# Kernel tuning notes

Measured on AMD Instinct MI355X. Metric: run time of the kernel, lower is better.

Reference implementation:

```python
import jax, jax.numpy as jnp
import numpy as np

NUM_CLASSES = 80
STRIDES = (8, 16, 32)


def _decode(p, stride):
    # p: [B, 5+C, H, W] raw head -> [B, HW, 5+C] decoded (xy in px, wh=exp*stride)
    B, C, H, W = p.shape
    ys, xs = jnp.meshgrid(jnp.arange(H), jnp.arange(W), indexing='ij')
    grid = jnp.stack([xs, ys], -1).reshape(H * W, 2).astype(p.dtype)
    out = p.reshape(B, C, H * W).transpose(0, 2, 1)
    xy = (out[..., :2] + grid) * stride
    wh = jnp.exp(out[..., 2:4]) * stride
    out = jnp.concatenate([xy, wh, out[..., 4:]], -1)
    es = jnp.full((H * W,), float(stride), p.dtype)
    return out, grid[:, 0], grid[:, 1], es


def _pairwise_iou(gt, pr):
    # gt [G,4] cxcywh, pr [A,4] -> [G,A]
    gt_tl = gt[:, None, :2] - gt[:, None, 2:] * 0.5
    gt_br = gt[:, None, :2] + gt[:, None, 2:] * 0.5
    pr_tl = pr[None, :, :2] - pr[None, :, 2:] * 0.5
    pr_br = pr[None, :, :2] + pr[None, :, 2:] * 0.5
    tl = jnp.maximum(gt_tl, pr_tl)
    br = jnp.minimum(gt_br, pr_br)
    en = jnp.all(tl < br, -1).astype(gt.dtype)
    inter = jnp.prod(br - tl, -1) * en
    a_gt = jnp.prod(gt[:, 2:], -1)[:, None]
    a_pr = jnp.prod(pr[:, 2:], -1)[None, :]
    return inter / (a_gt + a_pr - inter + 1e-16)


def _assign(gt_boxes, gt_cls, bbox, clsp, objp, xg, yg, es):
    # SimOTA assignment for one image (all fixed-shape; non-candidate anchors
    # are masked out via huge cost instead of boolean gather).
    G = gt_boxes.shape[0]
    xc = (xg + 0.5) * es  # [A] anchor centers
    yc = (yg + 0.5) * es
    gl = gt_boxes[:, 0:1] - 0.5 * gt_boxes[:, 2:3]
    gr = gt_boxes[:, 0:1] + 0.5 * gt_boxes[:, 2:3]
    gt_ = gt_boxes[:, 1:2] - 0.5 * gt_boxes[:, 3:4]
    gb = gt_boxes[:, 1:2] + 0.5 * gt_boxes[:, 3:4]
    in_box = (xc[None] > gl) & (xc[None] < gr) & (yc[None] > gt_) & (yc[None] < gb)  # [G,A]
    r = 2.5 * es[None]
    in_ctr = ((xc[None] > gt_boxes[:, 0:1] - r) & (xc[None] < gt_boxes[:, 0:1] + r)
              & (yc[None] > gt_boxes[:, 1:2] - r) & (yc[None] < gt_boxes[:, 1:2] + r))
    fg_cand = jnp.any(in_box, 0) | jnp.any(in_ctr, 0)  # [A]
    in_both = in_box & in_ctr  # [G,A]

    ious = _pairwise_iou(gt_boxes, bbox)  # [G,A]
    ious_m = jnp.where(fg_cand[None, :], ious, 0.0)
    iou_cost = -jnp.log(ious_m + 1e-8)

    # pairwise cls BCE cost: bce(sqrt(sigmoid(cls)*sigmoid(obj)), onehot(gt)).sum(-1)
    p = jnp.sqrt(jax.nn.sigmoid(clsp) * jax.nn.sigmoid(objp[:, None]))  # [A,C]
    lp = jnp.maximum(jnp.log(p), -100.0)
    l1p = jnp.maximum(jnp.log1p(-p), -100.0)
    t = jax.nn.one_hot(gt_cls, NUM_CLASSES, dtype=p.dtype)  # [G,C]
    cls_cost = -(jnp.einsum('ac,gc->ga', lp - l1p, t) + jnp.sum(l1p, -1)[None, :])

    cost = (cls_cost + 3.0 * iou_cost
            + 1e5 * (~in_both).astype(p.dtype)
            + 1e9 * (~fg_cand)[None, :].astype(p.dtype))

    # dynamic-k: k_g = clamp(sum(top10 ious), min=1)
    topk_ious, _ = jax.lax.top_k(ious_m, 10)
    dyn_k = jnp.clip(topk_ious.sum(-1).astype(jnp.int32), 1, None)  # [G]
    rank = jnp.argsort(jnp.argsort(cost, axis=1), axis=1)  # rank of each anchor per gt
    matching = (rank < dyn_k[:, None]) & fg_cand[None, :]  # [G,A]
    # resolve anchors matched to multiple gts: keep min-cost gt
    multi = matching.sum(0) > 1
    best = jnp.argmin(cost, 0)
    matching = jnp.where(multi[None, :], jnp.arange(G)[:, None] == best[None, :], matching)

    fg = jnp.any(matching, 0)  # [A]
    matched_gt = jnp.argmax(matching, 0)  # [A]
    pred_iou = jnp.sum(matching * ious, 0)  # [A]
    matched_cls = gt_cls[matched_gt]
    return fg, matched_gt, pred_iou, matched_cls


def _giou_loss(b, g):
    tl = jnp.maximum(b[..., :2] - b[..., 2:] * 0.5, g[..., :2] - g[..., 2:] * 0.5)
    br = jnp.minimum(b[..., :2] + b[..., 2:] * 0.5, g[..., :2] + g[..., 2:] * 0.5)
    area_b = jnp.prod(b[..., 2:], -1)
    area_g = jnp.prod(g[..., 2:], -1)
    en = jnp.all(tl < br, -1).astype(b.dtype)
    inter = jnp.prod(br - tl, -1) * en
    union = area_b + area_g - inter
    iou = inter / (union + 1e-16)
    ctl = jnp.minimum(b[..., :2] - b[..., 2:] * 0.5, g[..., :2] - g[..., 2:] * 0.5)
    cbr = jnp.maximum(b[..., :2] + b[..., 2:] * 0.5, g[..., :2] + g[..., 2:] * 0.5)
    area_c = jnp.maximum(jnp.prod(cbr - ctl, -1), 1e-16)
    giou = iou - (area_c - union) / area_c
    return 1.0 - jnp.clip(giou, -1.0, 1.0)


def _bce_logits(x, t):
    return jnp.maximum(x, 0.0) - x * t + jnp.log1p(jnp.exp(-jnp.abs(x)))


def _forward(p8, p16, p32, labels):
    outs, xo, yo, eo = [], [], [], []
    for p, s in zip((p8, p16, p32), STRIDES):
        o, x, y, e = _decode(p, s)
        outs.append(o); xo.append(x); yo.append(y); eo.append(e)
    outputs = jnp.concatenate(outs, 1)  # [B, A, 5+C]
    xg = jnp.concatenate(xo); yg = jnp.concatenate(yo); es = jnp.concatenate(eo)

    bbox = outputs[..., :4]
    obj = outputs[..., 4]
    cls = outputs[..., 5:]
    gt_boxes = labels[..., :4]
    gt_cls = labels[..., 4].astype(jnp.int32)

    # assignment runs under no_grad in torch
    det = jax.lax.stop_gradient(outputs)
    fg, matched_gt, pred_iou, matched_cls = jax.vmap(
        lambda gb, gc, o: _assign(gb, gc, o[..., :4], o[..., 5:], o[..., 4], xg, yg, es)
    )(gt_boxes, gt_cls, det)

    fgf = fg.astype(outputs.dtype)  # [B,A]
    reg_t = jnp.take_along_axis(gt_boxes, matched_gt[..., None], axis=1)  # [B,A,4]
    cls_t = (jax.nn.one_hot(matched_cls, NUM_CLASSES, dtype=outputs.dtype)
             * pred_iou[..., None] * fgf[..., None])

    loss_iou = jnp.sum(_giou_loss(bbox, reg_t) * fgf)
    loss_obj = jnp.sum(_bce_logits(obj, fgf))
    loss_cls = jnp.sum(_bce_logits(cls, cls_t) * fgf[..., None])
    num_fg = jnp.maximum(jnp.sum(fgf), 1.0)
    return (5.0 * loss_iou + loss_obj + loss_cls) / num_fg


def setup_inputs() -> dict:
    key = jax.random.key(0)
    k1, k2, k3, k4, k5, k6 = jax.random.split(key, 6)
    B, NGT = 32, 20
    p8 = jax.random.normal(k1, (B, 5 + NUM_CLASSES, 80, 80), dtype=jnp.float32)
    p16 = jax.random.normal(k2, (B, 5 + NUM_CLASSES, 40, 40), dtype=jnp.float32)
    p32 = jax.random.normal(k3, (B, 5 + NUM_CLASSES, 20, 20), dtype=jnp.float32)
    cxy = jax.random.uniform(k4, (B, NGT, 2), dtype=jnp.float32, minval=32.0, maxval=608.0)
    wh = jax.random.uniform(k5, (B, NGT, 2), dtype=jnp.float32, minval=16.0, maxval=128.0)
    cls = jax.random.randint(k6, (B, NGT, 1), 0, NUM_CLASSES).astype(jnp.float32)
    labels = jnp.concatenate([cxy, wh, cls], -1)
    return {"p8": p8, "p16": p16, "p32": p32, "labels": labels}


def reference(p8, p16, p32, labels):
    return _forward(p8, p16, p32, labels)
```

## Files before the change

kernel.cpp:

```cpp
#include <hip/hip_runtime.h>
#include <cstdint>
#include <cstddef>

#define NA 8400
#define NAP 8448
#define NB 32
#define NG 20
#define NCL 80
#define NBLK 33
#define KC_BLKS 12

__device__ __forceinline__ float frcp(float x) { return __builtin_amdgcn_rcpf(x); }
__device__ __forceinline__ float bce0(float x) {
  return fmaxf(x, 0.0f) + __logf(1.0f + __expf(-fabsf(x)));
}

__device__ __forceinline__ void anchor_info(int a, const float* p8, const float* p16,
                                            const float* p32, int b, const float*& base,
                                            int& hw, int& HW, int& xg, int& yg, float& fs) {
  if (a < 6400)      { hw = a;        HW = 6400; xg = hw % 80; yg = hw / 80; fs = 8.f;
                       base = p8  + (size_t)b * 85 * 6400; }
  else if (a < 8000) { hw = a - 6400; HW = 1600; xg = hw % 40; yg = hw / 40; fs = 16.f;
                       base = p16 + (size_t)b * 85 * 1600; }
  else               { hw = a - 8000; HW = 400;  xg = hw % 20; yg = hw / 20; fs = 32.f;
                       base = p32 + (size_t)b * 85 * 400; }
}

__device__ __forceinline__ float iou_raw(float gx, float gy, float gw, float gh, float4 p) {
  float gtlx = gx - gw * 0.5f, gtly = gy - gh * 0.5f;
  float gbrx = gx + gw * 0.5f, gbry = gy + gh * 0.5f;
  float ptlx = p.x - p.z * 0.5f, ptly = p.y - p.w * 0.5f;
  float pbrx = p.x + p.z * 0.5f, pbry = p.y + p.w * 0.5f;
  float tlx = fmaxf(gtlx, ptlx), tly = fmaxf(gtly, ptly);
  float brx = fminf(gbrx, pbrx), bry = fminf(gbry, pbry);
  float inter = ((tlx < brx) && (tly < bry)) ? (brx - tlx) * (bry - tly) : 0.0f;
  float ag = gw * gh, ap = p.z * p.w;
  return inter * frcp(ag + ap - inter + 1e-16f);
}

__device__ __forceinline__ float giou_loss(float4 bb, float gx, float gy, float gw, float gh) {
  float btlx = bb.x - bb.z * 0.5f, btly = bb.y - bb.w * 0.5f;
  float bbrx = bb.x + bb.z * 0.5f, bbry = bb.y + bb.w * 0.5f;
  float gtlx = gx - gw * 0.5f, gtly = gy - gh * 0.5f;
  float gbrx = gx + gw * 0.5f, gbry = gy + gh * 0.5f;
  float tlx = fmaxf(btlx, gtlx), tly = fmaxf(btly, gtly);
  float brx = fminf(bbrx, gbrx), bry = fminf(bbry, gbry);
  float area_b = bb.z * bb.w, area_g = gw * gh;
  float inter = ((tlx < brx) && (tly < bry)) ? (brx - tlx) * (bry - tly) : 0.0f;
  float uni = area_b + area_g - inter;
  float iou = inter / (uni + 1e-16f);
  float ctlx = fminf(btlx, gtlx), ctly = fminf(btly, gtly);
  float cbrx = fmaxf(bbrx, gbrx), cbry = fmaxf(bbry, gbry);
  float area_c = fmaxf((cbrx - ctlx) * (cbry - ctly), 1e-16f);
  float giou = iou - (area_c - uni) / area_c;
  giou = fminf(fmaxf(giou, -1.0f), 1.0f);
  return 1.0f - giou;
}

__device__ __forceinline__ void block_argmin(float& v, int& i, volatile float* s_v,
                                             volatile int* s_i, int tid) {
#pragma unroll
  for (int off = 32; off; off >>= 1) {
    float ov = __shfl_down(v, off, 64);
    int   oi = __shfl_down(i, off, 64);
    if (ov < v || (ov == v && oi < i)) { v = ov; i = oi; }
  }
  if ((tid & 63) == 0) { s_v[tid >> 6] = v; s_i[tid >> 6] = i; }
  __syncthreads();
  v = s_v[0]; i = s_i[0];
#pragma unroll
  for (int w = 1; w < 4; ++w) {
    float ov = s_v[w]; int oi = s_i[w];
    if (ov < v || (ov == v && oi < i)) { v = ov; i = oi; }
  }
}

__global__ __launch_bounds__(256) void kGXA(const float* __restrict__ p8,
                                            const float* __restrict__ p16,
                                            const float* __restrict__ p32,
                                            const float* __restrict__ labels,
                                            int* __restrict__ n_fg_cnt,
                                            int* __restrict__ fg_list,
                                            float4* __restrict__ bbox_c,
                                            float* __restrict__ sb_c,
                                            float* __restrict__ cost_tbl,
                                            float* __restrict__ iou_tbl,
                                            unsigned int* __restrict__ match_c,
                                            float* __restrict__ blk_obj) {
  __shared__ float s_gt[NG * 4];
  __shared__ int   s_gcls[NG];
  __shared__ int   s_a[256];
  __shared__ unsigned int s_msk[256];
  __shared__ float s_lso[256];
  __shared__ unsigned int s_wcnt[4];
  __shared__ float s_part[4];
  __shared__ unsigned int s_base;
  __shared__ int s_c;
  int blk = blockIdx.x, b = blockIdx.y, tid = threadIdx.x, lane = tid & 63, wid = tid >> 6;

  if (tid < NG) {
    s_gt[tid * 4 + 0] = labels[((size_t)b * NG + tid) * 5 + 0];
    s_gt[tid * 4 + 1] = labels[((size_t)b * NG + tid) * 5 + 1];
    s_gt[tid * 4 + 2] = labels[((size_t)b * NG + tid) * 5 + 2];
    s_gt[tid * 4 + 3] = labels[((size_t)b * NG + tid) * 5 + 3];
    s_gcls[tid] = (int)labels[((size_t)b * NG + tid) * 5 + 4];
  }
  __syncthreads();

  int a = blk * 256 + tid;
  match_c[(size_t)b * NAP + a] = 0u;

  bool fg = false;
  unsigned int msk = 0u;
  float bce_obj = 0.0f, obj = 0.0f;
  if (a < NA) {
    const float* base; int hw, HW, xg, yg; float fs;
    anchor_info(a, p8, p16, p32, b, base, hw, HW, xg, yg, fs);
    obj = base[4 * HW + hw];
    bce_obj = bce0(obj);
    float xc = ((float)xg + 0.5f) * fs;
    float yc = ((float)yg + 0.5f) * fs;
    float r = 2.5f * fs;
#pragma unroll
    for (int g = 0; g < NG; ++g) {
      float gx = s_gt[g * 4 + 0], gy = s_gt[g * 4 + 1];
      float gw = s_gt[g * 4 + 2], gh = s_gt[g * 4 + 3];
      bool inb = (xc > gx - 0.5f * gw) && (xc < gx + 0.5f * gw) &&
                 (yc > gy - 0.5f * gh) && (yc < gy + 0.5f * gh);
      bool inc = (xc > gx - r) && (xc < gx + r) && (yc > gy - r) && (yc < gy + r);
      fg = fg || inb || inc;
      if (inb && inc) msk |= (1u << g);
    }
  }

  unsigned long long bm = __ballot(fg);
#pragma unroll
  for (int off = 32; off; off >>= 1) bce_obj += __shfl_down(bce_obj, off, 64);
  if (lane == 0) { s_wcnt[wid] = (unsigned int)__popcll(bm); s_part[wid] = bce_obj; }
  __syncthreads();
  if (tid == 0) {
    unsigned int cnt = s_wcnt[0] + s_wcnt[1] + s_wcnt[2] + s_wcnt[3];
    s_c = (int)cnt;
    s_base = cnt ? (unsigned int)atomicAdd(&n_fg_cnt[b], (int)cnt) : 0u;
    blk_obj[b * NBLK + blk] = s_part[0] + s_part[1] + s_part[2] + s_part[3];
  }
  if (fg) {
    unsigned int li = 0;
    for (int w = 0; w < wid; ++w) li += s_wcnt[w];
    li += (unsigned int)__popcll(bm & ((1ull << lane) - 1ull));
    s_a[li] = a;
    s_msk[li] = msk;
    float uo = __logf(1.0f + __expf(-fabsf(obj)));
    s_lso[li] = fminf(obj, 0.0f) - uo;
  }
  __syncthreads();

  int c = s_c;
  if (tid >= c) return;
  int ci = (int)s_base + tid;
  size_t bo = (size_t)b * NAP;
  int aa = s_a[tid];
  unsigned int mk = s_msk[tid];
  float lso = s_lso[tid];

  const float* base; int hw, HW, xg, yg; float fs;
  anchor_info(aa, p8, p16, p32, b, base, hw, HW, xg, yg, fs);
  fg_list[bo + ci] = aa;

  float v0 = base[hw];
  float v1 = base[HW + hw];
  float v2 = base[2 * HW + hw];
  float v3 = base[3 * HW + hw];
  float4 pb = make_float4((v0 + (float)xg) * fs, (v1 + (float)yg) * fs,
                          __expf(v2) * fs, __expf(v3) * fs);
  bbox_c[bo + ci] = pb;

  float sl = 0.0f, sb = 0.0f;
  for (int cc = 0; cc < NCL; cc += 8) {
    float xs[8];
#pragma unroll
    for (int j = 0; j < 8; ++j) xs[j] = base[(5 + cc + j) * HW + hw];
#pragma unroll
    for (int j = 0; j < 8; ++j) {
      float x = xs[j];
      float u = __logf(1.0f + __expf(-fabsf(x)));
      sb += fmaxf(x, 0.0f) + u;
      float lsx = fminf(x, 0.0f) - u;
      float lpr = 0.5f * (lsx + lso);
      float p   = __expf(lpr);
      sl += fmaxf(__logf(1.0f - p), -100.0f);
    }
  }
  sb_c[bo + ci] = sb;

  for (int g = 0; g < NG; ++g) {
    int cg = s_gcls[g];
    float x = base[(5 + cg) * HW + hw];
    float u = __logf(1.0f + __expf(-fabsf(x)));
    float lsx = fminf(x, 0.0f) - u;
    float lpr = 0.5f * (lsx + lso);
    float p   = __expf(lpr);
    float l1p = fmaxf(__logf(1.0f - p), -100.0f);
    float wv  = fmaxf(lpr, -100.0f) - l1p;
    float iou = iou_raw(s_gt[g * 4 + 0], s_gt[g * 4 + 1], s_gt[g * 4 + 2], s_gt[g * 4 + 3], pb);
    float cst = -(wv + sl) - 3.0f * __logf(iou + 1e-8f);
    if (!((mk >> g) & 1u)) cst += 100000.0f;
    size_t row = ((size_t)b * NG + g) * NAP + ci;
    cost_tbl[row] = cst;
    iou_tbl[row]  = iou;
  }
}

__global__ __launch_bounds__(256) void kB(const float* __restrict__ cost_tbl,
                                          const float* __restrict__ iou_tbl,
                                          const int* __restrict__ n_fg,
                                          unsigned int* __restrict__ match_c) {
  __shared__ float s_cost[NAP];
  __shared__ float s_wt[4 * 10];
  __shared__ float s_v[4];
  __shared__ int   s_i[4];
  __shared__ int   s_k;

  int g = blockIdx.x, b = blockIdx.y, tid = threadIdx.x;
  int lane = tid & 63, wid = tid >> 6;
  int n = n_fg[b];
  size_t bo = (size_t)b * NAP;
  const float* __restrict__ cg = cost_tbl + ((size_t)b * NG + g) * NAP;
  const float* __restrict__ ig = iou_tbl  + ((size_t)b * NG + g) * NAP;

  float t10[10];
#pragma unroll
  for (int j = 0; j < 10; ++j) t10[j] = 0.0f;

  for (int ci = tid; ci < n; ci += 256) {
    float iou = ig[ci];
    float cst = cg[ci];
    if (iou > t10[9]) {
      t10[9] = iou;
#pragma unroll
      for (int q = 9; q > 0; --q) {
        if (t10[q] > t10[q - 1]) { float t = t10[q]; t10[q] = t10[q - 1]; t10[q - 1] = t; }
        else break;
      }
    }
    s_cost[ci] = cst;
  }

  for (int r = 0; r < 10; ++r) {
    float v = t10[0];
    float bv = v;
#pragma unroll
    for (int off = 32; off; off >>= 1) bv = fmaxf(bv, __shfl_down(bv, off, 64));
    bv = __shfl(bv, 0, 64);
    unsigned long long won = __ballot(v == bv);
    if (lane == __ffsll(won) - 1) {
#pragma unroll
      for (int q = 0; q < 9; ++q) t10[q] = t10[q + 1];
      t10[9] = -1.0f;
    }
    if (lane == 0) s_wt[wid * 10 + r] = bv;
  }
  __syncthreads();

  if (tid == 0) {
    int p0 = 0, p1 = 0, p2 = 0, p3 = 0;
    float s = 0.0f;
    for (int r = 0; r < 10; ++r) {
      float v0 = (p0 < 10) ? s_wt[p0]      : -2.0f;
      float v1 = (p1 < 10) ? s_wt[10 + p1] : -2.0f;
      float v2 = (p2 < 10) ? s_wt[20 + p2] : -2.0f;
      float v3 = (p3 < 10) ? s_wt[30 + p3] : -2.0f;
      float m = fmaxf(fmaxf(v0, v1), fmaxf(v2, v3));
      s += m;
      if (m == v0) ++p0; else if (m == v1) ++p1; else if (m == v2) ++p2; else ++p3;
    }
    int k = (int)s;
    if (k < 1) k = 1;
    s_k = k;
  }
  __syncthreads();
  int k = s_k;

  for (int it = 0; it < k; ++it) {
    float bv = 3.4e38f; int bi = NAP;
    for (int ci = tid; ci < n; ci += 256) {
      float v = s_cost[ci];
      if (v < bv || (v == bv && ci < bi)) { bv = v; bi = ci; }
    }
    block_argmin(bv, bi, s_v, s_i, tid);
    if (bv >= 1e8f) break;
    if (tid == 0) {
      atomicOr(&match_c[bo + bi], 1u << g);
      s_cost[bi] = 3.4e38f;
    }
    __syncthreads();
  }
}

__global__ __launch_bounds__(256) void kCD(const float* __restrict__ p8,
                                           const float* __restrict__ p16,
                                           const float* __restrict__ p32,
                                           const float* __restrict__ labels,
                                           const float4* __restrict__ bbox_c,
                                           const float* __restrict__ sb_c,
                                           const float* __restrict__ cost_tbl,
                                           const float* __restrict__ iou_tbl,
                                           const int* __restrict__ fg_list,
                                           const int* __restrict__ n_fg,
                                           const unsigned int* __restrict__ match_c,
                                           const float* __restrict__ blk_obj,
                                           float* __restrict__ accum,
                                           int* __restrict__ done_cnt,
                                           float* __restrict__ out) {
  __shared__ float s_gt[NG * 5];
  __shared__ float s_red[16];
  __shared__ int s_last;
  int b = blockIdx.y, tid = threadIdx.x;
  if (tid < NG * 5) s_gt[tid] = labels[(size_t)b * NG * 5 + tid];
  __syncthreads();

  int n = n_fg[b];
  size_t bo = (size_t)b * NAP;
  float li = 0.0f, oe = 0.0f, lc = 0.0f, nf = 0.0f;

  for (int ci = blockIdx.x * 256 + tid; ci < n; ci += KC_BLKS * 256) {
    unsigned int m = match_c[bo + ci];
    if (m == 0u) continue;
    int mg;
    if (m & (m - 1)) {
      float bestc = 3.4e38f; mg = 0;
#pragma unroll 4
      for (int g = 0; g < NG; ++g) {
        float cst = cost_tbl[((size_t)b * NG + g) * NAP + ci];
        if (cst < bestc) { bestc = cst; mg = g; }
      }
    } else {
      mg = __ffs(m) - 1;
    }
    int a = fg_list[bo + ci];
    const float* base; int hw, HW, xg, yg; float fs;
    anchor_info(a, p8, p16, p32, b, base, hw, HW, xg, yg, fs);
    float4 pb = bbox_c[bo + ci];
    float gx = s_gt[mg * 5], gy = s_gt[mg * 5 + 1];
    float gw = s_gt[mg * 5 + 2], gh = s_gt[mg * 5 + 3];
    int cg = (int)s_gt[mg * 5 + 4];
    float piou = iou_tbl[((size_t)b * NG + mg) * NAP + ci];
    li += giou_loss(pb, gx, gy, gw, gh);
    float xcls = base[(5 + cg) * HW + hw];
    lc += sb_c[bo + ci] - xcls * piou;
    oe += base[4 * HW + hw];
    nf += 1.0f;
  }

  float vals[4] = {li, oe, lc, nf};
#pragma unroll
  for (int q = 0; q < 4; ++q) {
#pragma unroll
    for (int off = 32; off; off >>= 1) vals[q] += __shfl_down(vals[q], off, 64);
  }
  if ((tid & 63) == 0) {
    int wid = tid >> 6;
    s_red[wid * 4 + 0] = vals[0];
    s_red[wid * 4 + 1] = vals[1];
    s_red[wid * 4 + 2] = vals[2];
    s_red[wid * 4 + 3] = vals[3];
  }
  __syncthreads();
  if (tid < 4) {
    const int slot[4] = {0, 2, 3, 4};
    float s = s_red[tid] + s_red[4 + tid] + s_red[8 + tid] + s_red[12 + tid];
    atomicAdd(&accum[slot[tid]], s);
  }

  if (tid == 0) {
    __threadfence();
    int old = atomicAdd(done_cnt, 1);
    s_last = (old == KC_BLKS * NB - 1) ? 1 : 0;
  }
  __syncthreads();
  if (s_last) {
    float s = 0.0f;
    for (int i = tid; i < NB * NBLK; i += 256) s += blk_obj[i];
#pragma unroll
    for (int off = 32; off; off >>= 1) s += __shfl_down(s, off, 64);
    if ((tid & 63) == 0) s_red[tid >> 6] = s;
    __syncthreads();
    if (tid == 0) {
      float obj_base = s_red[0] + s_red[1] + s_red[2] + s_red[3];
      float loss_iou = atomicAdd(&accum[0], 0.0f);
      float oex      = atomicAdd(&accum[2], 0.0f);
      float loss_cls = atomicAdd(&accum[3], 0.0f);
      float num_fg   = atomicAdd(&accum[4], 0.0f);
      float loss_obj = obj_base - oex;
      out[0] = (5.0f * loss_iou + loss_obj + loss_cls) / fmaxf(num_fg, 1.0f);
    }
  }
}

extern "C" void kernel_launch(void* const* d_in, const int* in_sizes, int n_in,
                              void* d_out, int out_size, void* d_ws, size_t ws_size,
                              hipStream_t stream) {
  const float* p8     = (const float*)d_in[0];
  const float* p16    = (const float*)d_in[1];
  const float* p32    = (const float*)d_in[2];
  const float* labels = (const float*)d_in[3];
  float* out = (float*)d_out;

  const size_t BAP = (size_t)NB * NAP;
  char* w = (char*)d_ws;
  float4*       bbox_c   = (float4*)w;
  float*        cost_tbl = (float*)(w + BAP * 16);
  float*        iou_tbl  = cost_tbl + (size_t)NB * NG * NAP;
  char*         w2       = (char*)(iou_tbl + (size_t)NB * NG * NAP);
  int*          fg_list  = (int*)(w2);
  unsigned int* match_c  = (unsigned int*)(w2 + BAP * 4);
  float*        sb_c     = (float*)(w2 + BAP * 8);
  char*         w3       = w2 + BAP * 12;
  int*          n_fg     = (int*)w3;
  float*        accum    = (float*)(w3 + 128);
  int*          done_cnt = (int*)(w3 + 160);
  float*        blk_obj  = (float*)(w3 + 256);

  hipMemsetAsync(w3, 0, 256, stream);

  kGXA<<<dim3(NBLK, NB), dim3(256), 0, stream>>>(p8, p16, p32, labels, n_fg, fg_list,
                                                 bbox_c, sb_c, cost_tbl, iou_tbl,
                                                 match_c, blk_obj);
  kB<<<dim3(NG, NB), dim3(256), 0, stream>>>(cost_tbl, iou_tbl, n_fg, match_c);
  kCD<<<dim3(KC_BLKS, NB), dim3(256), 0, stream>>>(p8, p16, p32, labels, bbox_c, sb_c,
                                                   cost_tbl, iou_tbl, fg_list, n_fg,
                                                   match_c, blk_obj, accum, done_cnt, out);
}
```

Baseline: 181.2 us.

## Split fused candidate kernel into compact, class-reduce and per-GT cost kernels

The single candidate-processing kernel is split into three. k1 compacts foreground anchors and stores bbox, log-sigmoid objectness and the in-box mask. k2 spreads the 80-class BCE sums over 8 thread groups per anchor and reduces them through shared memory. k3 computes the cost and IoU tables with one grid slice per ground truth. The aim is to remove load imbalance, since previously only the foreground threads of each block did all the class and GT work serially. The trade-off is two extra launches and extra global round-trips for the intermediate arrays.

```diff
diff --git a/kernel.cpp b/kernel.cpp
--- a/kernel.cpp
+++ b/kernel.cpp
@@ -75,27 +75,21 @@
   }
 }
 
-__global__ __launch_bounds__(256) void kGXA(const float* __restrict__ p8,
-                                            const float* __restrict__ p16,
-                                            const float* __restrict__ p32,
-                                            const float* __restrict__ labels,
-                                            int* __restrict__ n_fg_cnt,
-                                            int* __restrict__ fg_list,
-                                            float4* __restrict__ bbox_c,
-                                            float* __restrict__ sb_c,
-                                            float* __restrict__ cost_tbl,
-                                            float* __restrict__ iou_tbl,
-                                            unsigned int* __restrict__ match_c,
-                                            float* __restrict__ blk_obj) {
+__global__ __launch_bounds__(256) void k1(const float* __restrict__ p8,
+                                          const float* __restrict__ p16,
+                                          const float* __restrict__ p32,
+                                          const float* __restrict__ labels,
+                                          int* __restrict__ n_fg_cnt,
+                                          int* __restrict__ fg_list,
+                                          unsigned int* __restrict__ am_c,
+                                          float4* __restrict__ bbox_c,
+                                          float* __restrict__ lso_c,
+                                          unsigned int* __restrict__ match_c,
+                                          float* __restrict__ blk_obj) {
   __shared__ float s_gt[NG * 4];
-  __shared__ int   s_gcls[NG];
-  __shared__ int   s_a[256];
-  __shared__ unsigned int s_msk[256];
-  __shared__ float s_lso[256];
   __shared__ unsigned int s_wcnt[4];
   __shared__ float s_part[4];
   __shared__ unsigned int s_base;
-  __shared__ int s_c;
   int blk = blockIdx.x, b = blockIdx.y, tid = threadIdx.x, lane = tid & 63, wid = tid >> 6;
 
   if (tid < NG) {
@@ -103,7 +97,6 @@
     s_gt[tid * 4 + 1] = labels[((size_t)b * NG + tid) * 5 + 1];
     s_gt[tid * 4 + 2] = labels[((size_t)b * NG + tid) * 5 + 2];
     s_gt[tid * 4 + 3] = labels[((size_t)b * NG + tid) * 5 + 3];
-    s_gcls[tid] = (int)labels[((size_t)b * NG + tid) * 5 + 4];
   }
   __syncthreads();
 
@@ -113,8 +106,8 @@
   bool fg = false;
   unsigned int msk = 0u;
   float bce_obj = 0.0f, obj = 0.0f;
+  const float* base = nullptr; int hw = 0, HW = 0, xg = 0, yg = 0; float fs = 8.f;
   if (a < NA) {
-    const float* base; int hw, HW, xg, yg; float fs;
     anchor_info(a, p8, p16, p32, b, base, hw, HW, xg, yg, fs);
     obj = base[4 * HW + hw];
     bce_obj = bce0(obj);
@@ -140,74 +133,128 @@
   __syncthreads();
   if (tid == 0) {
     unsigned int cnt = s_wcnt[0] + s_wcnt[1] + s_wcnt[2] + s_wcnt[3];
-    s_c = (int)cnt;
     s_base = cnt ? (unsigned int)atomicAdd(&n_fg_cnt[b], (int)cnt) : 0u;
     blk_obj[b * NBLK + blk] = s_part[0] + s_part[1] + s_part[2] + s_part[3];
   }
-  if (fg) {
-    unsigned int li = 0;
-    for (int w = 0; w < wid; ++w) li += s_wcnt[w];
-    li += (unsigned int)__popcll(bm & ((1ull << lane) - 1ull));
-    s_a[li] = a;
-    s_msk[li] = msk;
-    float uo = __logf(1.0f + __expf(-fabsf(obj)));
-    s_lso[li] = fminf(obj, 0.0f) - uo;
-  }
-  __syncthreads();
-
-  int c = s_c;
-  if (tid >= c) return;
-  int ci = (int)s_base + tid;
+  __syncthreads();
+
+  if (!fg) return;
+  unsigned int pos = s_base;
+  for (int w = 0; w < wid; ++w) pos += s_wcnt[w];
+  pos += (unsigned int)__popcll(bm & ((1ull << lane) - 1ull));
   size_t bo = (size_t)b * NAP;
-  int aa = s_a[tid];
-  unsigned int mk = s_msk[tid];
-  float lso = s_lso[tid];
-
-  const float* base; int hw, HW, xg, yg; float fs;
-  anchor_info(aa, p8, p16, p32, b, base, hw, HW, xg, yg, fs);
-  fg_list[bo + ci] = aa;
+  int ci = (int)pos;
+  fg_list[bo + ci] = a;
+  am_c[bo + ci] = msk;
 
   float v0 = base[hw];
   float v1 = base[HW + hw];
   float v2 = base[2 * HW + hw];
   float v3 = base[3 * HW + hw];
-  float4 pb = make_float4((v0 + (float)xg) * fs, (v1 + (float)yg) * fs,
-                          __expf(v2) * fs, __expf(v3) * fs);
-  bbox_c[bo + ci] = pb;
-
-  float sl = 0.0f, sb = 0.0f;
-  for (int cc = 0; cc < NCL; cc += 8) {
-    float xs[8];
-#pragma unroll
-    for (int j = 0; j < 8; ++j) xs[j] = base[(5 + cc + j) * HW + hw];
-#pragma unroll
-    for (int j = 0; j < 8; ++j) {
-      float x = xs[j];
-      float u = __logf(1.0f + __expf(-fabsf(x)));
-      sb += fmaxf(x, 0.0f) + u;
-      float lsx = fminf(x, 0.0f) - u;
-      float lpr = 0.5f * (lsx + lso);
-      float p   = __expf(lpr);
-      sl += fmaxf(__logf(1.0f - p), -100.0f);
-    }
-  }
-  sb_c[bo + ci] = sb;
-
-  for (int g = 0; g < NG; ++g) {
-    int cg = s_gcls[g];
-    float x = base[(5 + cg) * HW + hw];
+  bbox_c[bo + ci] = make_float4((v0 + (float)xg) * fs, (v1 + (float)yg) * fs,
+                                __expf(v2) * fs, __expf(v3) * fs);
+  float uo = __logf(1.0f + __expf(-fabsf(obj)));
+  lso_c[bo + ci] = fminf(obj, 0.0f) - uo;
+}
+
+__global__ __launch_bounds__(256) void k2(const float* __restrict__ p8,
+                                          const float* __restrict__ p16,
+                                          const float* __restrict__ p32,
+                                          const int* __restrict__ fg_list,
+                                          const int* __restrict__ n_fg,
+                                          const float* __restrict__ lso_c,
+                                          float* __restrict__ sl_c,
+                                          float* __restrict__ sb_c) {
+  __shared__ float s_sl[8][33];
+  __shared__ float s_sb[8][33];
+  int b = blockIdx.y, tid = threadIdx.x;
+  int part = tid >> 5, cl = tid & 31;
+  int n = n_fg[b];
+  size_t bo = (size_t)b * NAP;
+
+  for (int base_ci = blockIdx.x * 32; base_ci < n; base_ci += gridDim.x * 32) {
+    int ci = base_ci + cl;
+    bool act = ci < n;
+    float sl = 0.0f, sb = 0.0f;
+    if (act) {
+      int a = fg_list[bo + ci];
+      float lso = lso_c[bo + ci];
+      const float* base; int hw, HW, xg, yg; float fs;
+      anchor_info(a, p8, p16, p32, b, base, hw, HW, xg, yg, fs);
+      const float* cb = base + (size_t)(5 + part * 10) * HW + hw;
+      float xs[10];
+#pragma unroll
+      for (int j = 0; j < 5; ++j) xs[j] = cb[j * HW];
+#pragma unroll
+      for (int j = 5; j < 10; ++j) xs[j] = cb[j * HW];
+#pragma unroll
+      for (int j = 0; j < 10; ++j) {
+        float x = xs[j];
+        float u = __logf(1.0f + __expf(-fabsf(x)));
+        sb += fmaxf(x, 0.0f) + u;
+        float lsx = fminf(x, 0.0f) - u;
+        float lpr = 0.5f * (lsx + lso);
+        float p   = __expf(lpr);
+        sl += fmaxf(__logf(1.0f - p), -100.0f);
+      }
+    }
+    s_sl[part][cl] = sl;
+    s_sb[part][cl] = sb;
+    __syncthreads();
+    if (tid < 32 && base_ci + tid < n) {
+      float tsl = 0.0f, tsb = 0.0f;
+#pragma unroll
+      for (int q = 0; q < 8; ++q) { tsl += s_sl[q][tid]; tsb += s_sb[q][tid]; }
+      sl_c[bo + base_ci + tid] = tsl;
+      sb_c[bo + base_ci + tid] = tsb;
+    }
+    __syncthreads();
+  }
+}
+
+__global__ __launch_bounds__(256) void k3(const float* __restrict__ p8,
+                                          const float* __restrict__ p16,
+                                          const float* __restrict__ p32,
+                                          const float* __restrict__ labels,
+                                          const int* __restrict__ fg_list,
+                                          const int* __restrict__ n_fg,
+                                          const float* __restrict__ lso_c,
+                                          const float* __restrict__ sl_c,
+                                          const float4* __restrict__ bbox_c,
+                                          const unsigned int* __restrict__ am_c,
+                                          float* __restrict__ cost_tbl,
+                                          float* __restrict__ iou_tbl) {
+  int g = blockIdx.y, b = blockIdx.z, tid = threadIdx.x;
+  int n = n_fg[b];
+  size_t bo = (size_t)b * NAP;
+  float gx = labels[((size_t)b * NG + g) * 5 + 0];
+  float gy = labels[((size_t)b * NG + g) * 5 + 1];
+  float gw = labels[((size_t)b * NG + g) * 5 + 2];
+  float gh = labels[((size_t)b * NG + g) * 5 + 3];
+  int   cg = (int)labels[((size_t)b * NG + g) * 5 + 4];
+  size_t row = ((size_t)b * NG + g) * NAP;
+
+  for (int ci = blockIdx.x * 256 + tid; ci < n; ci += gridDim.x * 256) {
+    int a = fg_list[bo + ci];
+    unsigned int am = am_c[bo + ci];
+    float lso = lso_c[bo + ci];
+    float sl  = sl_c[bo + ci];
+    float4 pb = bbox_c[bo + ci];
+    const float* base; int hw, HW, xg, yg; float fs;
+    anchor_info(a, p8, p16, p32, b, base, hw, HW, xg, yg, fs);
+    float x = base[(size_t)(5 + cg) * HW + hw];
+
     float u = __logf(1.0f + __expf(-fabsf(x)));
     float lsx = fminf(x, 0.0f) - u;
     float lpr = 0.5f * (lsx + lso);
     float p   = __expf(lpr);
     float l1p = fmaxf(__logf(1.0f - p), -100.0f);
     float wv  = fmaxf(lpr, -100.0f) - l1p;
-    float iou = iou_raw(s_gt[g * 4 + 0], s_gt[g * 4 + 1], s_gt[g * 4 + 2], s_gt[g * 4 + 3], pb);
+    float iou = iou_raw(gx, gy, gw, gh, pb);
     float cst = -(wv + sl) - 3.0f * __logf(iou + 1e-8f);
-    if (!((mk >> g) & 1u)) cst += 100000.0f;
-    size_t row = ((size_t)b * NG + g) * NAP + ci;
-    cost_tbl[row] = cst;
-    iou_tbl[row]  = iou;
+    if (!((am >> g) & 1u)) cst += 100000.0f;
+    cost_tbl[row + ci] = cst;
+    iou_tbl[row + ci]  = iou;
   }
 }
 
@@ -346,7 +393,7 @@
     int cg = (int)s_gt[mg * 5 + 4];
     float piou = iou_tbl[((size_t)b * NG + mg) * NAP + ci];
     li += giou_loss(pb, gx, gy, gw, gh);
-    float xcls = base[(5 + cg) * HW + hw];
+    float xcls = base[(size_t)(5 + cg) * HW + hw];
     lc += sb_c[bo + ci] - xcls * piou;
     oe += base[4 * HW + hw];
     nf += 1.0f;
@@ -415,7 +462,10 @@
   int*          fg_list  = (int*)(w2);
   unsigned int* match_c  = (unsigned int*)(w2 + BAP * 4);
   float*        sb_c     = (float*)(w2 + BAP * 8);
-  char*         w3       = w2 + BAP * 12;
+  float*        sl_c     = (float*)(w2 + BAP * 12);
+  float*        lso_c    = (float*)(w2 + BAP * 16);
+  unsigned int* am_c     = (unsigned int*)(w2 + BAP * 20);
+  char*         w3       = w2 + BAP * 24;
   int*          n_fg     = (int*)w3;
   float*        accum    = (float*)(w3 + 128);
   int*          done_cnt = (int*)(w3 + 160);
@@ -423,9 +473,11 @@
 
   hipMemsetAsync(w3, 0, 256, stream);
 
-  kGXA<<<dim3(NBLK, NB), dim3(256), 0, stream>>>(p8, p16, p32, labels, n_fg, fg_list,
-                                                 bbox_c, sb_c, cost_tbl, iou_tbl,
-                                                 match_c, blk_obj);
+  k1<<<dim3(NBLK, NB), dim3(256), 0, stream>>>(p8, p16, p32, labels, n_fg, fg_list, am_c,
+                                               bbox_c, lso_c, match_c, blk_obj);
+  k2<<<dim3(24, NB), dim3(256), 0, stream>>>(p8, p16, p32, fg_list, n_fg, lso_c, sl_c, sb_c);
+  k3<<<dim3(12, NG, NB), dim3(256), 0, stream>>>(p8, p16, p32, labels, fg_list, n_fg, lso_c,
+                                                 sl_c, bbox_c, am_c, cost_tbl, iou_tbl);
   kB<<<dim3(NG, NB), dim3(256), 0, stream>>>(cost_tbl, iou_tbl, n_fg, match_c);
   kCD<<<dim3(KC_BLKS, NB), dim3(256), 0, stream>>>(p8, p16, p32, labels, bbox_c, sb_c,
                                                    cost_tbl, iou_tbl, fg_list, n_fg,
```

Measured after the change: 173.4 us. 4.3% less time.
